# Kernel optimization log

Hardware: AMD Instinct MI355X
Metric: run time of the kernel (lower is better)

Reference implementation:

```python
import jax, jax.numpy as jnp
import numpy as np

B, S, D, H = 2, 2048, 1024, 16
HD = D // H
EPS = 1e-5


def setup_inputs() -> dict:
    key = jax.random.key(0)
    ks = jax.random.split(key, 8)
    std = 1.0 / np.sqrt(D)
    x = jax.random.normal(ks[0], (B, S, D), dtype=jnp.float32)
    # causal mask: True = attend (masked_fill where mask==0)
    attention_mask = jnp.tril(jnp.ones((S, S), dtype=bool))[None, None].repeat(B, axis=0)
    return {
        "x": x,
        "attention_mask": attention_mask,
        "ln_gamma": jnp.ones((D,), jnp.float32),
        "ln_beta": jnp.zeros((D,), jnp.float32),
        "w_qkv": jax.random.uniform(ks[1], (D, 3 * D), jnp.float32, -std, std),
        "b_qkv": jnp.zeros((3 * D,), jnp.float32),
        "w_gate": jax.random.uniform(ks[2], (D, D), jnp.float32, -std, std),
        "b_gate": jnp.zeros((D,), jnp.float32),
        "w_out": jax.random.uniform(ks[3], (D, D), jnp.float32, -std, std),
        "b_out": jnp.zeros((D,), jnp.float32),
        "rel_pos_bias": jnp.zeros((1, H, 1, 1), jnp.float32),
    }


def reference(x, attention_mask, ln_gamma, ln_beta, w_qkv, b_qkv,
              w_gate, b_gate, w_out, b_out, rel_pos_bias):
    # LayerNorm over model dim
    mu = jnp.mean(x, axis=-1, keepdims=True)
    var = jnp.mean(jnp.square(x - mu), axis=-1, keepdims=True)
    xn = (x - mu) * jax.lax.rsqrt(var + EPS) * ln_gamma + ln_beta

    qkv = xn @ w_qkv + b_qkv                      # [B,S,3D]
    qkv = qkv.reshape(B, S, 3, H, HD)
    q = qkv[:, :, 0].transpose(0, 2, 1, 3)        # [B,H,S,HD]
    k = qkv[:, :, 1].transpose(0, 2, 1, 3)
    v = qkv[:, :, 2].transpose(0, 2, 1, 3)

    u = jax.nn.silu(xn @ w_gate + b_gate)         # [B,S,D] SiLU gate

    scale = HD ** -0.5
    scores = jnp.einsum('bhqd,bhkd->bhqk', q * scale, k) + rel_pos_bias
    # masked_fill(mask==0, -inf) then sigmoid == zero out masked entries
    attn = jnp.where(attention_mask, jax.nn.sigmoid(scores), 0.0)
    ctx = jnp.einsum('bhqk,bhkd->bhqd', attn, v)  # [B,H,S,HD]
    ctx = ctx.transpose(0, 2, 1, 3).reshape(B, S, D)

    out = (ctx * u) @ w_out + b_out               # gated output proj
    return x + out                                # dropout=eval identity
```

## Files before the change

kernel.cpp:

```cpp
#include <hip/hip_runtime.h>
#include <hip/hip_bf16.h>
#include <cmath>

#define BB 2
#define SS 2048
#define DD 1024
#define HH 16
#define EPS 1e-5f
#define LOG2E 1.44269504088896f
#define QSCALE (0.125f * LOG2E)

typedef __attribute__((ext_vector_type(8))) short short8;
typedef __attribute__((ext_vector_type(4))) float f32x4;

__device__ inline unsigned short f2bf(float f) {
  union { float f; unsigned int u; } v; v.f = f;
  unsigned int u = v.u;
  unsigned int r = (u + 0x7FFFu + ((u >> 16) & 1u)) >> 16;
  return (unsigned short)r;
}
__device__ inline float bf2f(unsigned short h) {
  union { unsigned int u; float f; } v; v.u = ((unsigned int)h) << 16;
  return v.f;
}
__device__ inline unsigned short f2bf_fast(float f) {
  union { float f; unsigned int u; } v; v.f = f;
  return (unsigned short)((v.u + 0x8000u) >> 16);
}

__global__ __launch_bounds__(256) void ln_kernel(
    const float* __restrict__ x, const float* __restrict__ gamma,
    const float* __restrict__ beta, unsigned short* __restrict__ xn) {
  int row = blockIdx.x;
  int t = threadIdx.x;
  const float* xr = x + (size_t)row * DD;
  float4 v = *(const float4*)(xr + t * 4);
  float s = v.x + v.y + v.z + v.w;
  float sq = v.x * v.x + v.y * v.y + v.z * v.z + v.w * v.w;
  for (int off = 32; off > 0; off >>= 1) {
    s += __shfl_down(s, off, 64);
    sq += __shfl_down(sq, off, 64);
  }
  __shared__ float ls[4], lq[4];
  int wave = t >> 6, lane = t & 63;
  if (lane == 0) { ls[wave] = s; lq[wave] = sq; }
  __syncthreads();
  float tot = ls[0] + ls[1] + ls[2] + ls[3];
  float totq = lq[0] + lq[1] + lq[2] + lq[3];
  float mu = tot * (1.0f / DD);
  float var = totq * (1.0f / DD) - mu * mu;
  float rstd = rsqrtf(var + EPS);
  float4 g = *(const float4*)(gamma + t * 4);
  float4 bt = *(const float4*)(beta + t * 4);
  ushort4 o;
  o.x = f2bf((v.x - mu) * rstd * g.x + bt.x);
  o.y = f2bf((v.y - mu) * rstd * g.y + bt.y);
  o.z = f2bf((v.z - mu) * rstd * g.z + bt.z);
  o.w = f2bf((v.w - mu) * rstd * g.w + bt.w);
  *(ushort4*)(xn + (size_t)row * DD + t * 4) = o;
}

__global__ __launch_bounds__(256) void wtrans(
    const float* __restrict__ W, unsigned short* __restrict__ Wt,
    int K, int N) {
  __shared__ unsigned short tile[32][33];
  int bx = blockIdx.x * 32;
  int by = blockIdx.y * 32;
  int tx = threadIdx.x & 31, ty = threadIdx.x >> 5;
#pragma unroll
  for (int i = 0; i < 32; i += 8)
    tile[ty + i][tx] = f2bf(W[(size_t)(by + ty + i) * N + bx + tx]);
  __syncthreads();
#pragma unroll
  for (int i = 0; i < 32; i += 8)
    Wt[(size_t)(bx + ty + i) * K + by + tx] = tile[tx][ty + i];
}

__global__ __launch_bounds__(256) void gemm_qkvg(
    const unsigned short* __restrict__ A, const unsigned short* __restrict__ Bt,
    const float* __restrict__ bqkv, const float* __restrict__ bgate,
    unsigned short* __restrict__ qkb, unsigned short* __restrict__ vTb,
    unsigned short* __restrict__ ub) {
  __shared__ unsigned short As[128 * 32];
  __shared__ unsigned short Bs[128 * 32];
  const int K = 1024;
  int tid = threadIdx.x;
  int wave = tid >> 6, lane = tid & 63;
  int quad = lane >> 4, m16 = lane & 15;
  int wm = wave >> 1, wn = wave & 1;
  int m0 = blockIdx.y * 128, n0 = blockIdx.x * 128;

  int lrow = tid >> 2;
  int lcol = (tid & 3) * 8;

  f32x4 acc[4][4];
#pragma unroll
  for (int i = 0; i < 4; ++i)
#pragma unroll
    for (int j = 0; j < 4; ++j) acc[i][j] = (f32x4){0.f, 0.f, 0.f, 0.f};

  for (int k0 = 0; k0 < K; k0 += 32) {
    uint4 a0 = *(const uint4*)(A + (size_t)(m0 + lrow) * K + k0 + lcol);
    uint4 a1 = *(const uint4*)(A + (size_t)(m0 + lrow + 64) * K + k0 + lcol);
    uint4 b0 = *(const uint4*)(Bt + (size_t)(n0 + lrow) * K + k0 + lcol);
    uint4 b1 = *(const uint4*)(Bt + (size_t)(n0 + lrow + 64) * K + k0 + lcol);
    __syncthreads();
    *(uint4*)&As[lrow * 32 + lcol] = a0;
    *(uint4*)&As[(lrow + 64) * 32 + lcol] = a1;
    *(uint4*)&Bs[lrow * 32 + lcol] = b0;
    *(uint4*)&Bs[(lrow + 64) * 32 + lcol] = b1;
    __syncthreads();
    short8 af[4], bfr[4];
#pragma unroll
    for (int mi = 0; mi < 4; ++mi)
      af[mi] = *(const short8*)&As[(wm * 64 + mi * 16 + m16) * 32 + quad * 8];
#pragma unroll
    for (int ni = 0; ni < 4; ++ni)
      bfr[ni] = *(const short8*)&Bs[(wn * 64 + ni * 16 + m16) * 32 + quad * 8];
#pragma unroll
    for (int mi = 0; mi < 4; ++mi)
#pragma unroll
      for (int ni = 0; ni < 4; ++ni)
        acc[mi][ni] = __builtin_amdgcn_mfma_f32_16x16x32_bf16(
            af[mi], bfr[ni], acc[mi][ni], 0, 0, 0);
  }

  int nwin = n0 + wn * 64;
  int sec = nwin >> 10;
  if (sec <= 1) {
    float qs = (sec == 0) ? QSCALE : 1.0f;
#pragma unroll
    for (int ni = 0; ni < 4; ++ni) {
      int col = nwin + ni * 16 + m16;
      float bb = bqkv[col];
#pragma unroll
      for (int mi = 0; mi < 4; ++mi)
#pragma unroll
        for (int r = 0; r < 4; ++r) {
          int row = m0 + wm * 64 + mi * 16 + quad * 4 + r;
          qkb[(size_t)row * 2048 + col] = f2bf((acc[mi][ni][r] + bb) * qs);
        }
    }
  } else if (sec == 2) {
#pragma unroll
    for (int ni = 0; ni < 4; ++ni) {
      int col = nwin + ni * 16 + m16;
      float bb = bqkv[col];
      int vcol = col - 2048;
      int hh = vcol >> 6, dd = vcol & 63;
#pragma unroll
      for (int mi = 0; mi < 4; ++mi) {
        int row0 = m0 + wm * 64 + mi * 16 + quad * 4;
        int bat = row0 >> 11, s0 = row0 & 2047;
        ushort4 o;
        o.x = f2bf(acc[mi][ni][0] + bb);
        o.y = f2bf(acc[mi][ni][1] + bb);
        o.z = f2bf(acc[mi][ni][2] + bb);
        o.w = f2bf(acc[mi][ni][3] + bb);
        *(ushort4*)&vTb[(size_t)((bat * 16 + hh) * 64 + dd) * 2048 + s0] = o;
      }
    }
  } else {
#pragma unroll
    for (int ni = 0; ni < 4; ++ni) {
      int col = nwin + ni * 16 + m16;
      int g = col - 3072;
      float bb = bgate[g];
#pragma unroll
      for (int mi = 0; mi < 4; ++mi)
#pragma unroll
        for (int r = 0; r < 4; ++r) {
          int row = m0 + wm * 64 + mi * 16 + quad * 4 + r;
          float v = acc[mi][ni][r] + bb;
          v = v * __builtin_amdgcn_rcpf(1.0f + exp2f(-v * LOG2E));
          ub[(size_t)row * 1024 + g] = f2bf(v);
        }
    }
  }
}

__global__ __launch_bounds__(256) void gemm_out(
    const unsigned short* __restrict__ A, const unsigned short* __restrict__ Bt,
    const float* __restrict__ bias, const float* __restrict__ resid,
    float* __restrict__ C) {
  __shared__ unsigned short As[128 * 32];
  __shared__ unsigned short Bs[128 * 32];
  const int K = 1024, N = 1024;
  int tid = threadIdx.x;
  int wave = tid >> 6, lane = tid & 63;
  int quad = lane >> 4, m16 = lane & 15;
  int wm = wave >> 1, wn = wave & 1;
  int m0 = blockIdx.y * 128, n0 = blockIdx.x * 128;
  int lrow = tid >> 2;
  int lcol = (tid & 3) * 8;

  f32x4 acc[4][4];
#pragma unroll
  for (int i = 0; i < 4; ++i)
#pragma unroll
    for (int j = 0; j < 4; ++j) acc[i][j] = (f32x4){0.f, 0.f, 0.f, 0.f};

  for (int k0 = 0; k0 < K; k0 += 32) {
    uint4 a0 = *(const uint4*)(A + (size_t)(m0 + lrow) * K + k0 + lcol);
    uint4 a1 = *(const uint4*)(A + (size_t)(m0 + lrow + 64) * K + k0 + lcol);
    uint4 b0 = *(const uint4*)(Bt + (size_t)(n0 + lrow) * K + k0 + lcol);
    uint4 b1 = *(const uint4*)(Bt + (size_t)(n0 + lrow + 64) * K + k0 + lcol);
    __syncthreads();
    *(uint4*)&As[lrow * 32 + lcol] = a0;
    *(uint4*)&As[(lrow + 64) * 32 + lcol] = a1;
    *(uint4*)&Bs[lrow * 32 + lcol] = b0;
    *(uint4*)&Bs[(lrow + 64) * 32 + lcol] = b1;
    __syncthreads();
    short8 af[4], bfr[4];
#pragma unroll
    for (int mi = 0; mi < 4; ++mi)
      af[mi] = *(const short8*)&As[(wm * 64 + mi * 16 + m16) * 32 + quad * 8];
#pragma unroll
    for (int ni = 0; ni < 4; ++ni)
      bfr[ni] = *(const short8*)&Bs[(wn * 64 + ni * 16 + m16) * 32 + quad * 8];
#pragma unroll
    for (int mi = 0; mi < 4; ++mi)
#pragma unroll
      for (int ni = 0; ni < 4; ++ni)
        acc[mi][ni] = __builtin_amdgcn_mfma_f32_16x16x32_bf16(
            af[mi], bfr[ni], acc[mi][ni], 0, 0, 0);
  }
#pragma unroll
  for (int ni = 0; ni < 4; ++ni) {
    int col = n0 + wn * 64 + ni * 16 + m16;
    float bb = bias[col];
#pragma unroll
    for (int mi = 0; mi < 4; ++mi)
#pragma unroll
      for (int r = 0; r < 4; ++r) {
        int row = m0 + wm * 64 + mi * 16 + quad * 4 + r;
        C[(size_t)row * N + col] =
            acc[mi][ni][r] + bb + resid[(size_t)row * N + col];
      }
  }
}

__global__ __launch_bounds__(256) void attn_mfma(
    const unsigned short* __restrict__ qk, const unsigned short* __restrict__ vT,
    const unsigned short* __restrict__ u, const float* __restrict__ rpb,
    unsigned short* __restrict__ prod) {
  __shared__ unsigned short Qs[64][72];
  __shared__ unsigned short Ks[64][72];
  __shared__ unsigned short Vt[64][72];
  __shared__ unsigned short Ps[64][72];

  int qt = gridDim.x - 1 - blockIdx.x;
  int q0 = qt * 64;
  int bh = blockIdx.y;
  int b = bh >> 4, h = bh & 15;
  int t = threadIdx.x;
  int wave = t >> 6, lane = t & 63;
  int quad = lane >> 4, m16 = lane & 15;

  const unsigned short* qbase = qk + (size_t)(b * SS) * 2048 + h * 64;
  const unsigned short* kbase = qbase + 1024;
  const unsigned short* vbase = vT + (size_t)(bh * 64) * 2048;

  {
    int row = t >> 3, blk = t & 7;
    const unsigned short* s0 = qbase + (size_t)(q0 + row) * 2048 + blk * 8;
    *(uint4*)&Qs[row][blk * 8] = *(const uint4*)s0;
    *(uint4*)&Qs[row + 32][blk * 8] = *(const uint4*)(s0 + (size_t)32 * 2048);
  }

  f32x4 zero4 = {0.f, 0.f, 0.f, 0.f};
  f32x4 cacc[4];
#pragma unroll
  for (int nb = 0; nb < 4; ++nb) cacc[nb] = zero4;

  float hb2 = rpb[h] * LOG2E;
  int ntiles = qt + 1;

  for (int kt = 0; kt < ntiles; ++kt) {
    int k0 = kt * 64;
    bool diag = (kt == qt);
    int row = t >> 3, blk = t & 7;
    const unsigned short* ks = kbase + (size_t)(k0 + row) * 2048 + blk * 8;
    uint4 k0v = *(const uint4*)ks;
    uint4 k1v = *(const uint4*)(ks + (size_t)32 * 2048);
    const unsigned short* vs = vbase + (size_t)row * 2048 + k0 + blk * 8;
    uint4 v0v = *(const uint4*)vs;
    uint4 v1v = *(const uint4*)(vs + (size_t)32 * 2048);
    __syncthreads();
    *(uint4*)&Ks[row][blk * 8] = k0v;
    *(uint4*)&Ks[row + 32][blk * 8] = k1v;
    *(uint4*)&Vt[row][blk * 8] = v0v;
    *(uint4*)&Vt[row + 32][blk * 8] = v1v;
    __syncthreads();

    f32x4 sacc[4];
#pragma unroll
    for (int nb = 0; nb < 4; ++nb) sacc[nb] = zero4;
#pragma unroll
    for (int s = 0; s < 2; ++s) {
      short8 a = *(const short8*)&Qs[wave * 16 + m16][s * 32 + quad * 8];
#pragma unroll
      for (int nb = 0; nb < 4; ++nb) {
        short8 bf = *(const short8*)&Ks[nb * 16 + m16][s * 32 + quad * 8];
        sacc[nb] = __builtin_amdgcn_mfma_f32_16x16x32_bf16(a, bf, sacc[nb], 0, 0, 0);
      }
    }

#pragma unroll
    for (int nb = 0; nb < 4; ++nb) {
#pragma unroll
      for (int r = 0; r < 4; ++r) {
        float y = sacc[nb][r] + hb2;
        float p = __builtin_amdgcn_rcpf(1.0f + exp2f(-y));
        if (diag) {
          int key = k0 + nb * 16 + m16;
          int q = q0 + wave * 16 + quad * 4 + r;
          if (key > q) p = 0.f;
        }
        Ps[wave * 16 + quad * 4 + r][nb * 16 + m16] = f2bf_fast(p);
      }
    }

#pragma unroll
    for (int s = 0; s < 2; ++s) {
      short8 a = *(const short8*)&Ps[wave * 16 + m16][s * 32 + quad * 8];
#pragma unroll
      for (int nb = 0; nb < 4; ++nb) {
        short8 bf = *(const short8*)&Vt[nb * 16 + m16][s * 32 + quad * 8];
        cacc[nb] = __builtin_amdgcn_mfma_f32_16x16x32_bf16(a, bf, cacc[nb], 0, 0, 0);
      }
    }
  }

  const unsigned short* ub_ = u + (size_t)(b * SS) * 1024 + h * 64;
  unsigned short* pb_ = prod + (size_t)(b * SS) * 1024 + h * 64;
#pragma unroll
  for (int nb = 0; nb < 4; ++nb) {
    int d = nb * 16 + m16;
#pragma unroll
    for (int r = 0; r < 4; ++r) {
      int q = q0 + wave * 16 + quad * 4 + r;
      float uv = bf2f(ub_[(size_t)q * 1024 + d]);
      pb_[(size_t)q * 1024 + d] = f2bf(cacc[nb][r] * uv);
    }
  }
}

extern "C" void kernel_launch(void* const* d_in, const int* in_sizes, int n_in,
                              void* d_out, int out_size, void* d_ws, size_t ws_size,
                              hipStream_t stream) {
  const float* x      = (const float*)d_in[0];
  const float* gamma  = (const float*)d_in[2];
  const float* beta   = (const float*)d_in[3];
  const float* w_qkv  = (const float*)d_in[4];
  const float* b_qkv  = (const float*)d_in[5];
  const float* w_gate = (const float*)d_in[6];
  const float* b_gate = (const float*)d_in[7];
  const float* w_out  = (const float*)d_in[8];
  const float* b_out  = (const float*)d_in[9];
  const float* rpb    = (const float*)d_in[10];
  float* out = (float*)d_out;

  unsigned short* xnb   = (unsigned short*)d_ws;
  unsigned short* qkb   = xnb + 4194304;
  unsigned short* vTb   = qkb + 8388608;
  unsigned short* ub    = vTb + 4194304;
  unsigned short* prodb = ub + 4194304;
  unsigned short* wcatT = prodb + 4194304;
  unsigned short* woutT = wcatT + 4194304;

  ln_kernel<<<BB * SS, 256, 0, stream>>>(x, gamma, beta, xnb);
  wtrans<<<dim3(3072 / 32, 1024 / 32), 256, 0, stream>>>(w_qkv, wcatT, 1024, 3072);
  wtrans<<<dim3(1024 / 32, 1024 / 32), 256, 0, stream>>>(w_gate, wcatT + (size_t)3072 * 1024, 1024, 1024);
  wtrans<<<dim3(1024 / 32, 1024 / 32), 256, 0, stream>>>(w_out, woutT, 1024, 1024);
  gemm_qkvg<<<dim3(4096 / 128, 4096 / 128), 256, 0, stream>>>(
      xnb, wcatT, b_qkv, b_gate, qkb, vTb, ub);
  attn_mfma<<<dim3(SS / 64, BB * HH), 256, 0, stream>>>(qkb, vTb, ub, rpb, prodb);
  gemm_out<<<dim3(1024 / 128, 4096 / 128), 256, 0, stream>>>(
      prodb, woutT, b_out, x, out);
}
```

Before: 281.0 us.

## Pair causal query tiles per attention block and prefetch GEMM tiles into registers

```diff
diff --git a/kernel.cpp b/kernel.cpp
--- a/kernel.cpp
+++ b/kernel.cpp
@@ -92,6 +92,10 @@
 
   int lrow = tid >> 2;
   int lcol = (tid & 3) * 8;
+  const unsigned short* Ar0 = A + (size_t)(m0 + lrow) * K + lcol;
+  const unsigned short* Ar1 = A + (size_t)(m0 + lrow + 64) * K + lcol;
+  const unsigned short* Br0 = Bt + (size_t)(n0 + lrow) * K + lcol;
+  const unsigned short* Br1 = Bt + (size_t)(n0 + lrow + 64) * K + lcol;
 
   f32x4 acc[4][4];
 #pragma unroll
@@ -99,17 +103,24 @@
 #pragma unroll
     for (int j = 0; j < 4; ++j) acc[i][j] = (f32x4){0.f, 0.f, 0.f, 0.f};
 
+  uint4 a0 = *(const uint4*)Ar0;
+  uint4 a1 = *(const uint4*)Ar1;
+  uint4 b0 = *(const uint4*)Br0;
+  uint4 b1 = *(const uint4*)Br1;
+
   for (int k0 = 0; k0 < K; k0 += 32) {
-    uint4 a0 = *(const uint4*)(A + (size_t)(m0 + lrow) * K + k0 + lcol);
-    uint4 a1 = *(const uint4*)(A + (size_t)(m0 + lrow + 64) * K + k0 + lcol);
-    uint4 b0 = *(const uint4*)(Bt + (size_t)(n0 + lrow) * K + k0 + lcol);
-    uint4 b1 = *(const uint4*)(Bt + (size_t)(n0 + lrow + 64) * K + k0 + lcol);
     __syncthreads();
     *(uint4*)&As[lrow * 32 + lcol] = a0;
     *(uint4*)&As[(lrow + 64) * 32 + lcol] = a1;
     *(uint4*)&Bs[lrow * 32 + lcol] = b0;
     *(uint4*)&Bs[(lrow + 64) * 32 + lcol] = b1;
     __syncthreads();
+    if (k0 + 32 < K) {
+      a0 = *(const uint4*)(Ar0 + k0 + 32);
+      a1 = *(const uint4*)(Ar1 + k0 + 32);
+      b0 = *(const uint4*)(Br0 + k0 + 32);
+      b1 = *(const uint4*)(Br1 + k0 + 32);
+    }
     short8 af[4], bfr[4];
 #pragma unroll
     for (int mi = 0; mi < 4; ++mi)
@@ -193,6 +204,10 @@
   int m0 = blockIdx.y * 128, n0 = blockIdx.x * 128;
   int lrow = tid >> 2;
   int lcol = (tid & 3) * 8;
+  const unsigned short* Ar0 = A + (size_t)(m0 + lrow) * K + lcol;
+  const unsigned short* Ar1 = A + (size_t)(m0 + lrow + 64) * K + lcol;
+  const unsigned short* Br0 = Bt + (size_t)(n0 + lrow) * K + lcol;
+  const unsigned short* Br1 = Bt + (size_t)(n0 + lrow + 64) * K + lcol;
 
   f32x4 acc[4][4];
 #pragma unroll
@@ -200,17 +215,24 @@
 #pragma unroll
     for (int j = 0; j < 4; ++j) acc[i][j] = (f32x4){0.f, 0.f, 0.f, 0.f};
 
+  uint4 a0 = *(const uint4*)Ar0;
+  uint4 a1 = *(const uint4*)Ar1;
+  uint4 b0 = *(const uint4*)Br0;
+  uint4 b1 = *(const uint4*)Br1;
+
   for (int k0 = 0; k0 < K; k0 += 32) {
-    uint4 a0 = *(const uint4*)(A + (size_t)(m0 + lrow) * K + k0 + lcol);
-    uint4 a1 = *(const uint4*)(A + (size_t)(m0 + lrow + 64) * K + k0 + lcol);
-    uint4 b0 = *(const uint4*)(Bt + (size_t)(n0 + lrow) * K + k0 + lcol);
-    uint4 b1 = *(const uint4*)(Bt + (size_t)(n0 + lrow + 64) * K + k0 + lcol);
     __syncthreads();
     *(uint4*)&As[lrow * 32 + lcol] = a0;
     *(uint4*)&As[(lrow + 64) * 32 + lcol] = a1;
     *(uint4*)&Bs[lrow * 32 + lcol] = b0;
     *(uint4*)&Bs[(lrow + 64) * 32 + lcol] = b1;
     __syncthreads();
+    if (k0 + 32 < K) {
+      a0 = *(const uint4*)(Ar0 + k0 + 32);
+      a1 = *(const uint4*)(Ar1 + k0 + 32);
+      b0 = *(const uint4*)(Br0 + k0 + 32);
+      b1 = *(const uint4*)(Br1 + k0 + 32);
+    }
     short8 af[4], bfr[4];
 #pragma unroll
     for (int mi = 0; mi < 4; ++mi)
@@ -244,13 +266,14 @@
     const unsigned short* __restrict__ qk, const unsigned short* __restrict__ vT,
     const unsigned short* __restrict__ u, const float* __restrict__ rpb,
     unsigned short* __restrict__ prod) {
-  __shared__ unsigned short Qs[64][72];
-  __shared__ unsigned short Ks[64][72];
-  __shared__ unsigned short Vt[64][72];
-  __shared__ unsigned short Ps[64][72];
-
-  int qt = gridDim.x - 1 - blockIdx.x;
-  int q0 = qt * 64;
+  __shared__ unsigned short Qs[128 * 72];
+  __shared__ unsigned short Ks[64 * 72];
+  __shared__ unsigned short Vs[64 * 72];
+  __shared__ unsigned short Ps[64 * 72];
+
+  int qtA = blockIdx.x;
+  int qtB = 31 - qtA;
+  int q0A = qtA * 64, q0B = qtB * 64;
   int bh = blockIdx.y;
   int b = bh >> 4, h = bh & 15;
   int t = threadIdx.x;
@@ -259,75 +282,84 @@
 
   const unsigned short* qbase = qk + (size_t)(b * SS) * 2048 + h * 64;
   const unsigned short* kbase = qbase + 1024;
-  const unsigned short* vbase = vT + (size_t)(bh * 64) * 2048;
+  const unsigned short* vbase = vT + (size_t)bh * 64 * 2048;
+
+  int row = t >> 3, blk8 = (t & 7) * 8;
 
   {
-    int row = t >> 3, blk = t & 7;
-    const unsigned short* s0 = qbase + (size_t)(q0 + row) * 2048 + blk * 8;
-    *(uint4*)&Qs[row][blk * 8] = *(const uint4*)s0;
-    *(uint4*)&Qs[row + 32][blk * 8] = *(const uint4*)(s0 + (size_t)32 * 2048);
+    const unsigned short* sA = qbase + (size_t)(q0A + row) * 2048 + blk8;
+    const unsigned short* sB = qbase + (size_t)(q0B + row) * 2048 + blk8;
+    *(uint4*)&Qs[row * 72 + blk8] = *(const uint4*)sA;
+    *(uint4*)&Qs[(row + 32) * 72 + blk8] = *(const uint4*)(sA + (size_t)32 * 2048);
+    *(uint4*)&Qs[(row + 64) * 72 + blk8] = *(const uint4*)sB;
+    *(uint4*)&Qs[(row + 96) * 72 + blk8] = *(const uint4*)(sB + (size_t)32 * 2048);
   }
 
   f32x4 zero4 = {0.f, 0.f, 0.f, 0.f};
-  f32x4 cacc[4];
-#pragma unroll
-  for (int nb = 0; nb < 4; ++nb) cacc[nb] = zero4;
+  f32x4 caccA[4], caccB[4];
+#pragma unroll
+  for (int nb = 0; nb < 4; ++nb) { caccA[nb] = zero4; caccB[nb] = zero4; }
 
   float hb2 = rpb[h] * LOG2E;
-  int ntiles = qt + 1;
-
-  for (int kt = 0; kt < ntiles; ++kt) {
+  int ktmax = qtB;
+
+  for (int kt = 0; kt <= ktmax; ++kt) {
     int k0 = kt * 64;
-    bool diag = (kt == qt);
-    int row = t >> 3, blk = t & 7;
-    const unsigned short* ks = kbase + (size_t)(k0 + row) * 2048 + blk * 8;
-    uint4 k0v = *(const uint4*)ks;
-    uint4 k1v = *(const uint4*)(ks + (size_t)32 * 2048);
-    const unsigned short* vs = vbase + (size_t)row * 2048 + k0 + blk * 8;
-    uint4 v0v = *(const uint4*)vs;
-    uint4 v1v = *(const uint4*)(vs + (size_t)32 * 2048);
-    __syncthreads();
-    *(uint4*)&Ks[row][blk * 8] = k0v;
-    *(uint4*)&Ks[row + 32][blk * 8] = k1v;
-    *(uint4*)&Vt[row][blk * 8] = v0v;
-    *(uint4*)&Vt[row + 32][blk * 8] = v1v;
-    __syncthreads();
-
-    f32x4 sacc[4];
-#pragma unroll
-    for (int nb = 0; nb < 4; ++nb) sacc[nb] = zero4;
-#pragma unroll
-    for (int s = 0; s < 2; ++s) {
-      short8 a = *(const short8*)&Qs[wave * 16 + m16][s * 32 + quad * 8];
+    const unsigned short* kp = kbase + (size_t)(k0 + row) * 2048 + blk8;
+    const unsigned short* vp = vbase + (size_t)row * 2048 + k0 + blk8;
+    uint4 kv0 = *(const uint4*)kp;
+    uint4 kv1 = *(const uint4*)(kp + (size_t)32 * 2048);
+    uint4 vv0 = *(const uint4*)vp;
+    uint4 vv1 = *(const uint4*)(vp + (size_t)32 * 2048);
+    __syncthreads();
+    *(uint4*)&Ks[row * 72 + blk8] = kv0;
+    *(uint4*)&Ks[(row + 32) * 72 + blk8] = kv1;
+    *(uint4*)&Vs[row * 72 + blk8] = vv0;
+    *(uint4*)&Vs[(row + 32) * 72 + blk8] = vv1;
+    __syncthreads();
+
+#pragma unroll
+    for (int tile = 0; tile < 2; ++tile) {
+      if (tile == 1 && kt > qtA) break;
+      int qlds = (tile == 0) ? (64 + wave * 16) : (wave * 16);
+      int q0 = (tile == 0) ? q0B : q0A;
+      bool diag = (tile == 0) ? (kt == qtB) : (kt == qtA);
+      f32x4* cacc = (tile == 0) ? caccB : caccA;
+
+      f32x4 sacc[4];
+#pragma unroll
+      for (int nb = 0; nb < 4; ++nb) sacc[nb] = zero4;
+#pragma unroll
+      for (int s = 0; s < 2; ++s) {
+        short8 a = *(const short8*)&Qs[(qlds + m16) * 72 + s * 32 + quad * 8];
+#pragma unroll
+        for (int nb = 0; nb < 4; ++nb) {
+          short8 bf = *(const short8*)&Ks[(nb * 16 + m16) * 72 + s * 32 + quad * 8];
+          sacc[nb] = __builtin_amdgcn_mfma_f32_16x16x32_bf16(a, bf, sacc[nb], 0, 0, 0);
+        }
+      }
 #pragma unroll
       for (int nb = 0; nb < 4; ++nb) {
-        short8 bf = *(const short8*)&Ks[nb * 16 + m16][s * 32 + quad * 8];
-        sacc[nb] = __builtin_amdgcn_mfma_f32_16x16x32_bf16(a, bf, sacc[nb], 0, 0, 0);
+#pragma unroll
+        for (int r = 0; r < 4; ++r) {
+          float y = sacc[nb][r] + hb2;
+          float p = __builtin_amdgcn_rcpf(1.0f + exp2f(-y));
+          if (diag) {
+            int key = k0 + nb * 16 + m16;
+            int q = q0 + wave * 16 + quad * 4 + r;
+            if (key > q) p = 0.f;
+          }
+          Ps[(wave * 16 + quad * 4 + r) * 72 + nb * 16 + m16] = f2bf_fast(p);
+        }
       }
-    }
-
-#pragma unroll
-    for (int nb = 0; nb < 4; ++nb) {
-#pragma unroll
-      for (int r = 0; r < 4; ++r) {
-        float y = sacc[nb][r] + hb2;
-        float p = __builtin_amdgcn_rcpf(1.0f + exp2f(-y));
-        if (diag) {
-          int key = k0 + nb * 16 + m16;
-          int q = q0 + wave * 16 + quad * 4 + r;
-          if (key > q) p = 0.f;
+#pragma unroll
+      for (int s = 0; s < 2; ++s) {
+        short8 a = *(const short8*)&Ps[(wave * 16 + m16) * 72 + s * 32 + quad * 8];
+#pragma unroll
+        for (int nb = 0; nb < 4; ++nb) {
+          short8 bf = *(const short8*)&Vs[(nb * 16 + m16) * 72 + s * 32 + quad * 8];
+          cacc[nb] = __builtin_amdgcn_mfma_f32_16x16x32_bf16(a, bf, cacc[nb], 0, 0, 0);
         }
-        Ps[wave * 16 + quad * 4 + r][nb * 16 + m16] = f2bf_fast(p);
-      }
-    }
-
-#pragma unroll
-    for (int s = 0; s < 2; ++s) {
-      short8 a = *(const short8*)&Ps[wave * 16 + m16][s * 32 + quad * 8];
-#pragma unroll
-      for (int nb = 0; nb < 4; ++nb) {
-        short8 bf = *(const short8*)&Vt[nb * 16 + m16][s * 32 + quad * 8];
-        cacc[nb] = __builtin_amdgcn_mfma_f32_16x16x32_bf16(a, bf, cacc[nb], 0, 0, 0);
       }
     }
   }
@@ -339,9 +371,10 @@
     int d = nb * 16 + m16;
 #pragma unroll
     for (int r = 0; r < 4; ++r) {
-      int q = q0 + wave * 16 + quad * 4 + r;
-      float uv = bf2f(ub_[(size_t)q * 1024 + d]);
-      pb_[(size_t)q * 1024 + d] = f2bf(cacc[nb][r] * uv);
+      int qA = q0A + wave * 16 + quad * 4 + r;
+      int qB = q0B + wave * 16 + quad * 4 + r;
+      pb_[(size_t)qA * 1024 + d] = f2bf(caccA[nb][r] * bf2f(ub_[(size_t)qA * 1024 + d]));
+      pb_[(size_t)qB * 1024 + d] = f2bf(caccB[nb][r] * bf2f(ub_[(size_t)qB * 1024 + d]));
     }
   }
 }
@@ -375,7 +408,7 @@
   wtrans<<<dim3(1024 / 32, 1024 / 32), 256, 0, stream>>>(w_out, woutT, 1024, 1024);
   gemm_qkvg<<<dim3(4096 / 128, 4096 / 128), 256, 0, stream>>>(
       xnb, wcatT, b_qkv, b_gate, qkb, vTb, ub);
-  attn_mfma<<<dim3(SS / 64, BB * HH), 256, 0, stream>>>(qkb, vTb, ub, rpb, prodb);
+  attn_mfma<<<dim3(16, BB * HH), 256, 0, stream>>>(qkb, vTb, ub, rpb, prodb);
   gemm_out<<<dim3(1024 / 128, 4096 / 128), 256, 0, stream>>>(
       prodb, woutT, b_out, x, out);
 }
```

Measured after the change: 254.2 us. 1.11x faster.
